# Kernel tuning notes

Measured on AMD Instinct MI355X. Metric: run time of the kernel, lower is better.

Reference implementation:

```python
import jax, jax.numpy as jnp
import numpy as np

N, D, V = 2048, 64, 2048


def setup_inputs() -> dict:
    key = jax.random.key(0)
    k_ids, k_emb, k_tree, k_map = jax.random.split(key, 4)
    language_ids = jax.random.randint(k_ids, (N,), 0, V)
    language_embeddings = jax.random.normal(k_emb, (N, D), dtype=jnp.float32)
    # symmetric distance tables, mimicking the symmetric try/except dict lookup
    t = jax.random.uniform(k_tree, (V, V), dtype=jnp.float32)
    tree_dist = (t + t.T) * 0.5
    m = jax.random.uniform(k_map, (V, V), dtype=jnp.float32)
    map_dist = (m + m.T) * 0.5
    return {
        "language_ids": language_ids,
        "language_embeddings": language_embeddings,
        "tree_dist": tree_dist,
        "map_dist": map_dist,
    }


def reference(language_ids, language_embeddings, tree_dist, map_dist):
    # pairwise mean-L1 distance between embeddings: [N, N]
    emb_dist = jnp.mean(
        jnp.abs(language_embeddings[:, None, :] - language_embeddings[None, :, :]),
        axis=-1,
    )
    # largest_value_map_dist as computed in __init__
    largest = jnp.max(map_dist)
    ii = language_ids[:, None]  # [N, 1]
    jj = language_ids[None, :]  # [1, N]
    metric = (tree_dist[ii, jj] + map_dist[ii, jj] / largest) * 0.5  # [N, N]
    # pairs with equal language ids are skipped in the original loop
    mask = (ii != jj).astype(emb_dist.dtype)
    per_pair = jnp.abs(emb_dist - metric) * mask
    return jnp.sum(per_pair) / jnp.sum(mask)
```

## Files before the change

kernel.cpp:

```cpp
#include <hip/hip_runtime.h>
#include <hip/hip_bf16.h>

#define NL 2048
#define DE 64
#define VV 2048
#define BI 64
#define BJ 32
#define NTI (NL / BI)
#define NTJ (NL / BJ)
#define NBLK 1056
#define STI 66
#define STJ 36


__global__ __launch_bounds__(1024) void prep_kernel(const int* __restrict__ ids,
                                                    const float4* __restrict__ m4,
                                                    float* __restrict__ pmax,
                                                    int* __restrict__ perm,
                                                    int* __restrict__ sids) {
    const int t = threadIdx.x;
    const int lane = t & 63, wave = t >> 6;
    const int b = blockIdx.x;

    if (b < 256) {
        const float4* p = m4 + (size_t)b * 4096;
        const float4 x0 = p[t], x1 = p[t + 1024], x2 = p[t + 2048], x3 = p[t + 3072];
        float v = fmaxf(fmaxf(fmaxf(x0.x, x0.y), fmaxf(x0.z, x0.w)),
                        fmaxf(fmaxf(x1.x, x1.y), fmaxf(x1.z, x1.w)));
        v = fmaxf(v, fmaxf(fmaxf(x2.x, x2.y), fmaxf(x2.z, x2.w)));
        v = fmaxf(v, fmaxf(fmaxf(x3.x, x3.y), fmaxf(x3.z, x3.w)));
        #pragma unroll
        for (int o = 32; o > 0; o >>= 1)
            v = fmaxf(v, __shfl_down(v, o));
        __shared__ float wl[16];
        if (lane == 0) wl[wave] = v;
        __syncthreads();
        if (t == 0) {
            float m = wl[0];
            #pragma unroll
            for (int i = 1; i < 16; ++i) m = fmaxf(m, wl[i]);
            pmax[b] = m;
        }
    } else {
        __shared__ unsigned hist[VV];
        __shared__ unsigned offs[VV];
        __shared__ unsigned wtot[16];
        __shared__ unsigned wexc[16];
        hist[2 * t] = 0u; hist[2 * t + 1] = 0u;
        __syncthreads();
        const int id0 = ids[2 * t], id1 = ids[2 * t + 1];
        atomicAdd(&hist[id0], 1u);
        atomicAdd(&hist[id1], 1u);
        __syncthreads();
        const unsigned h0 = hist[2 * t], h1 = hist[2 * t + 1];
        const unsigned s = h0 + h1;
        unsigned ps = s;
        #pragma unroll
        for (int o = 1; o < 64; o <<= 1) {
            unsigned u = __shfl_up(ps, o);
            if (lane >= o) ps += u;
        }
        if (lane == 63) wtot[wave] = ps;
        __syncthreads();
        if (wave == 0 && lane < 16) {
            unsigned v = wtot[lane];
            unsigned pv = v;
            #pragma unroll
            for (int o = 1; o < 16; o <<= 1) {
                unsigned u = __shfl_up(pv, o);
                if (lane >= o) pv += u;
            }
            wexc[lane] = pv - v;
        }
        __syncthreads();
        const unsigned ex = wexc[wave] + ps - s;
        offs[2 * t]     = ex;
        offs[2 * t + 1] = ex + h0;
        __syncthreads();
        unsigned p0 = atomicAdd(&offs[id0], 1u);
        perm[p0] = 2 * t;     sids[p0] = id0;
        unsigned p1 = atomicAdd(&offs[id1], 1u);
        perm[p1] = 2 * t + 1; sids[p1] = id1;
    }
}

__global__ __launch_bounds__(512, 8) void loss_kernel(
    const float* __restrict__ emb,
    const float* __restrict__ tree, const float* __restrict__ mapd,
    const int* __restrict__ perm, const int* __restrict__ sids,
    const float* __restrict__ pmax,
    float* __restrict__ psum, unsigned* __restrict__ pcnt)
{
    const int t = threadIdx.x;

    const int L = blockIdx.x;
    int bi = (int)((65.0f - sqrtf(4225.0f - 4.0f * (float)L)) * 0.5f);
    if (bi > NTI - 1) bi = NTI - 1;
    if (bi < 0) bi = 0;
    while (65 * bi - bi * bi > L) --bi;
    while (65 * (bi + 1) - (bi + 1) * (bi + 1) <= L) ++bi;
    const int bj = 2 * bi + (L - (65 * bi - bi * bi));

    const int i0 = (t >> 4) * 2;
    const int j0 = (t & 15) * 2;

    int ia[2], ja[2];
    ia[0] = sids[bi * BI + i0];     ia[1] = sids[bi * BI + i0 + 1];
    ja[0] = sids[bj * BJ + j0];     ja[1] = sids[bj * BJ + j0 + 1];
    float tg[2][2], mg[2][2];
    #pragma unroll
    for (int s = 0; s < 2; ++s)
        #pragma unroll
        for (int c = 0; c < 2; ++c) {
            const int off = ia[s] * VV + ja[c];
            tg[s][c] = tree[off];
            mg[s][c] = mapd[off];
        }

    __shared__ __align__(16) float Eit[DE][STI];
    __shared__ __align__(16) float Ejt[DE][STJ];
    __shared__ float wm[8];

    float pv = pmax[t & 255];

    {
        const int r  = t & 63;
        const int c0 = (t >> 6) << 3;
        const int gi = perm[bi * BI + r];
        const float4* pa = (const float4*)(emb + (size_t)gi * DE + c0);
        float4 a0 = pa[0], a1 = pa[1];
        Eit[c0 + 0][r] = a0.x; Eit[c0 + 1][r] = a0.y; Eit[c0 + 2][r] = a0.z; Eit[c0 + 3][r] = a0.w;
        Eit[c0 + 4][r] = a1.x; Eit[c0 + 5][r] = a1.y; Eit[c0 + 6][r] = a1.z; Eit[c0 + 7][r] = a1.w;

        const int rj  = t & 31;
        const int cj0 = (t >> 5) << 2;
        const int gj = perm[bj * BJ + rj];
        const float4* pb = (const float4*)(emb + (size_t)gj * DE + cj0);
        float4 b0 = pb[0];
        Ejt[cj0 + 0][rj] = b0.x; Ejt[cj0 + 1][rj] = b0.y; Ejt[cj0 + 2][rj] = b0.z; Ejt[cj0 + 3][rj] = b0.w;
    }
    #pragma unroll
    for (int o = 32; o > 0; o >>= 1)
        pv = fmaxf(pv, __shfl_down(pv, o));
    if ((t & 63) == 0) wm[t >> 6] = pv;
    __syncthreads();

    float bm = fmaxf(fmaxf(wm[0], wm[1]), fmaxf(wm[2], wm[3]));
    bm = fmaxf(bm, fmaxf(fmaxf(wm[4], wm[5]), fmaxf(wm[6], wm[7])));
    const float inv = 1.0f / bm;

    float acc[2][2];
    acc[0][0] = 0.0f; acc[0][1] = 0.0f; acc[1][0] = 0.0f; acc[1][1] = 0.0f;

    #pragma unroll 2
    for (int k = 0; k < 16; ++k) {
        #pragma unroll
        for (int q = 0; q < 4; ++q) {
            const int d = 4 * k + q;
            const float2 a = *(const float2*)&Eit[d][i0];
            const float2 b = *(const float2*)&Ejt[d][j0];
            acc[0][0] += fabsf(a.x - b.x); acc[0][1] += fabsf(a.x - b.y);
            acc[1][0] += fabsf(a.y - b.x); acc[1][1] += fabsf(a.y - b.y);
        }
    }

    float pp = 0.0f;
    unsigned cnt = 0;
    #pragma unroll
    for (int s = 0; s < 2; ++s) {
        const int posi = bi * BI + i0 + s;
        #pragma unroll
        for (int c = 0; c < 2; ++c) {
            const int posj = bj * BJ + j0 + c;
            if (posi < posj && ia[s] != ja[c]) {
                const float metric = (tg[s][c] + mg[s][c] * inv) * 0.5f;
                pp += 2.0f * fabsf(acc[s][c] * (1.0f / (float)DE) - metric);
                cnt += 2u;
            }
        }
    }

    #pragma unroll
    for (int o = 32; o > 0; o >>= 1) {
        pp  += __shfl_down(pp, o);
        cnt += __shfl_down(cnt, o);
    }
    __shared__ float    wsum_l[8];
    __shared__ unsigned wcnt_l[8];
    if ((t & 63) == 0) { wsum_l[t >> 6] = pp; wcnt_l[t >> 6] = cnt; }
    __syncthreads();
    if (t == 0) {
        float    S = 0.0f;
        unsigned C = 0u;
        #pragma unroll
        for (int w = 0; w < 8; ++w) { S += wsum_l[w]; C += wcnt_l[w]; }
        psum[L] = S;
        pcnt[L] = C;
    }
}

__global__ __launch_bounds__(1024) void finalize_kernel(const float* __restrict__ psum,
                                                        const unsigned* __restrict__ pcnt,
                                                        float* __restrict__ out) {
    const int t = threadIdx.x;
    const int lane = t & 63, wave = t >> 6;
    double s = 0.0;
    unsigned c = 0;
    for (int i = t; i < NBLK; i += 1024) { s += (double)psum[i]; c += pcnt[i]; }
    #pragma unroll
    for (int o = 32; o > 0; o >>= 1) {
        s += __shfl_down(s, o);
        c += __shfl_down(c, o);
    }
    __shared__ double   sl[16];
    __shared__ unsigned cl[16];
    if (lane == 0) { sl[wave] = s; cl[wave] = c; }
    __syncthreads();
    if (t == 0) {
        double   S = sl[0];
        unsigned C = cl[0];
        #pragma unroll
        for (int i = 1; i < 16; ++i) { S += sl[i]; C += cl[i]; }
        out[0] = (float)(S / (double)C);
    }
}

extern "C" void kernel_launch(void* const* d_in, const int* in_sizes, int n_in,
                              void* d_out, int out_size, void* d_ws, size_t ws_size,
                              hipStream_t stream) {
    const int*   ids  = (const int*)d_in[0];
    const float* emb  = (const float*)d_in[1];
    const float* tree = (const float*)d_in[2];
    const float* mapd = (const float*)d_in[3];
    float* out = (float*)d_out;

    float*    pmax = (float*)d_ws;
    int*      perm = (int*)((char*)d_ws + 1024);
    int*      sids = (int*)((char*)d_ws + 9216);
    float*    psum = (float*)((char*)d_ws + 17408);
    unsigned* pcnt = (unsigned*)((char*)d_ws + 21632);

    prep_kernel<<<257, 1024, 0, stream>>>(ids, (const float4*)mapd, pmax, perm, sids);

    loss_kernel<<<NBLK, 512, 0, stream>>>(emb, tree, mapd, perm, sids, pmax, psum, pcnt);

    finalize_kernel<<<1, 1024, 0, stream>>>(psum, pcnt, out);
}
```

Before: 98.86 us.

## Use square 64x64 tiles with 2x4 per-thread register blocking in loss kernel

Changes the loss kernel's tile from 64x32 to 64x64. There are now 528 upper-triangular blocks instead of 1056, and the block-index decode is rewritten to match. Each thread computes a 2x4 output micro-tile using float4 LDS reads. This should raise arithmetic intensity per shared-memory load and halve per-block setup overhead. In exchange, each thread holds more registers, and fewer blocks means less parallelism across the 256 CUs.

```diff
diff --git a/kernel.cpp b/kernel.cpp
--- a/kernel.cpp
+++ b/kernel.cpp
@@ -5,12 +5,11 @@
 #define DE 64
 #define VV 2048
 #define BI 64
-#define BJ 32
-#define NTI (NL / BI)
-#define NTJ (NL / BJ)
-#define NBLK 1056
+#define BJ 64
+#define NT 32
+#define NBLK 528
 #define STI 66
-#define STJ 36
+#define STJ 68
 
 
 __global__ __launch_bounds__(1024) void prep_kernel(const int* __restrict__ ids,
@@ -84,7 +83,7 @@
     }
 }
 
-__global__ __launch_bounds__(512, 8) void loss_kernel(
+__global__ __launch_bounds__(512, 6) void loss_kernel(
     const float* __restrict__ emb,
     const float* __restrict__ tree, const float* __restrict__ mapd,
     const int* __restrict__ perm, const int* __restrict__ sids,
@@ -94,24 +93,25 @@
     const int t = threadIdx.x;
 
     const int L = blockIdx.x;
-    int bi = (int)((65.0f - sqrtf(4225.0f - 4.0f * (float)L)) * 0.5f);
-    if (bi > NTI - 1) bi = NTI - 1;
+    int bi = (int)((65.0f - sqrtf(4225.0f - 8.0f * (float)L)) * 0.5f);
+    if (bi > NT - 1) bi = NT - 1;
     if (bi < 0) bi = 0;
-    while (65 * bi - bi * bi > L) --bi;
-    while (65 * (bi + 1) - (bi + 1) * (bi + 1) <= L) ++bi;
-    const int bj = 2 * bi + (L - (65 * bi - bi * bi));
+    while (bi * (65 - bi) / 2 > L) --bi;
+    while ((bi + 1) * (64 - bi) / 2 <= L) ++bi;
+    const int bj = bi + (L - bi * (65 - bi) / 2);
 
     const int i0 = (t >> 4) * 2;
-    const int j0 = (t & 15) * 2;
-
-    int ia[2], ja[2];
+    const int j0 = (t & 15) * 4;
+
+    int ia[2], ja[4];
     ia[0] = sids[bi * BI + i0];     ia[1] = sids[bi * BI + i0 + 1];
-    ja[0] = sids[bj * BJ + j0];     ja[1] = sids[bj * BJ + j0 + 1];
-    float tg[2][2], mg[2][2];
+    #pragma unroll
+    for (int c = 0; c < 4; ++c) ja[c] = sids[bj * BJ + j0 + c];
+    float tg[2][4], mg[2][4];
     #pragma unroll
     for (int s = 0; s < 2; ++s)
         #pragma unroll
-        for (int c = 0; c < 2; ++c) {
+        for (int c = 0; c < 4; ++c) {
             const int off = ia[s] * VV + ja[c];
             tg[s][c] = tree[off];
             mg[s][c] = mapd[off];
@@ -132,12 +132,11 @@
         Eit[c0 + 0][r] = a0.x; Eit[c0 + 1][r] = a0.y; Eit[c0 + 2][r] = a0.z; Eit[c0 + 3][r] = a0.w;
         Eit[c0 + 4][r] = a1.x; Eit[c0 + 5][r] = a1.y; Eit[c0 + 6][r] = a1.z; Eit[c0 + 7][r] = a1.w;
 
-        const int rj  = t & 31;
-        const int cj0 = (t >> 5) << 2;
-        const int gj = perm[bj * BJ + rj];
-        const float4* pb = (const float4*)(emb + (size_t)gj * DE + cj0);
-        float4 b0 = pb[0];
-        Ejt[cj0 + 0][rj] = b0.x; Ejt[cj0 + 1][rj] = b0.y; Ejt[cj0 + 2][rj] = b0.z; Ejt[cj0 + 3][rj] = b0.w;
+        const int gj = perm[bj * BJ + r];
+        const float4* pb = (const float4*)(emb + (size_t)gj * DE + c0);
+        float4 b0 = pb[0], b1 = pb[1];
+        Ejt[c0 + 0][r] = b0.x; Ejt[c0 + 1][r] = b0.y; Ejt[c0 + 2][r] = b0.z; Ejt[c0 + 3][r] = b0.w;
+        Ejt[c0 + 4][r] = b1.x; Ejt[c0 + 5][r] = b1.y; Ejt[c0 + 6][r] = b1.z; Ejt[c0 + 7][r] = b1.w;
     }
     #pragma unroll
     for (int o = 32; o > 0; o >>= 1)
@@ -149,8 +148,11 @@
     bm = fmaxf(bm, fmaxf(fmaxf(wm[4], wm[5]), fmaxf(wm[6], wm[7])));
     const float inv = 1.0f / bm;
 
-    float acc[2][2];
-    acc[0][0] = 0.0f; acc[0][1] = 0.0f; acc[1][0] = 0.0f; acc[1][1] = 0.0f;
+    float acc[2][4];
+    #pragma unroll
+    for (int s = 0; s < 2; ++s)
+        #pragma unroll
+        for (int c = 0; c < 4; ++c) acc[s][c] = 0.0f;
 
     #pragma unroll 2
     for (int k = 0; k < 16; ++k) {
@@ -158,9 +160,11 @@
         for (int q = 0; q < 4; ++q) {
             const int d = 4 * k + q;
             const float2 a = *(const float2*)&Eit[d][i0];
-            const float2 b = *(const float2*)&Ejt[d][j0];
+            const float4 b = *(const float4*)&Ejt[d][j0];
             acc[0][0] += fabsf(a.x - b.x); acc[0][1] += fabsf(a.x - b.y);
+            acc[0][2] += fabsf(a.x - b.z); acc[0][3] += fabsf(a.x - b.w);
             acc[1][0] += fabsf(a.y - b.x); acc[1][1] += fabsf(a.y - b.y);
+            acc[1][2] += fabsf(a.y - b.z); acc[1][3] += fabsf(a.y - b.w);
         }
     }
 
@@ -170,7 +174,7 @@
     for (int s = 0; s < 2; ++s) {
         const int posi = bi * BI + i0 + s;
         #pragma unroll
-        for (int c = 0; c < 2; ++c) {
+        for (int c = 0; c < 4; ++c) {
             const int posj = bj * BJ + j0 + c;
             if (posi < posj && ia[s] != ja[c]) {
                 const float metric = (tg[s][c] + mg[s][c] * inv) * 0.5f;
```

Result: slower. 104.2 us (+5.4%).
